# Kernel tuning notes

Hardware: AMD Instinct MI355X
Metric: run time of the kernel (lower is better)

The kernel has to match this reference:

```python
import jax, jax.numpy as jnp
import numpy as np

H = 4          # num_heads
DK = 128       # head_k_dim = hidden*expand_k/H = 1024*0.5/4
DV = 256       # head_v_dim = hidden*expand_v/H
LOW_RANK = 16  # gate_low_rank_dim
GATE_NORM = 16.0  # gate_logit_normalizer
CHUNK = 64
EPS = 1e-5


def setup_inputs() -> dict:
    key = jax.random.key(0)
    ks = jax.random.split(key, 10)
    Dm = 1024
    Kd, Vd = H * DK, H * DV  # key_dim=512, value_dim=1024
    def lin(k, fan_in, fan_out):
        return jax.random.normal(k, (fan_in, fan_out), jnp.float32) * (fan_in ** -0.5)
    return {
        "x": jax.random.normal(ks[0], (4, 2048, Dm), jnp.float32),
        "Wq": lin(ks[1], Dm, Kd),
        "Wk": lin(ks[2], Dm, Kd),
        "Wv": lin(ks[3], Dm, Vd),
        "Wg": lin(ks[4], Dm, Vd),            # output gate proj
        "Wgk1": lin(ks[5], Dm, LOW_RANK),     # low-rank gate proj (no bias)
        "Wgk2": lin(ks[6], LOW_RANK, Kd),     # second gate proj (with bias)
        "bgk2": jnp.zeros((Kd,), jnp.float32),
        "Wo": lin(ks[7], Vd, Dm),
        "gnw": jnp.ones((DV,), jnp.float32),  # FusedRMSNormGated weight
    }


def _gla_chunk(q, k, v, gk):
    """Exact chunkwise evaluation of the GLA recurrence:
       S_t = diag(exp(gk_t)) S_{t-1} + k_t^T v_t;  o_t = scale * q_t S_t.
       q,k,gk: [B,T,H,DK], v: [B,T,H,DV]."""
    B, T, _, _ = q.shape
    NC, C = T // CHUNK, CHUNK
    scale = DK ** -0.5
    def chunks(a):  # [B,T,H,D] -> [NC,B,H,C,D]
        return a.reshape(B, NC, C, H, a.shape[-1]).transpose(1, 0, 3, 2, 4)
    qc, kc, vc, gc = chunks(q), chunks(k), chunks(v), chunks(gk)
    G = jnp.cumsum(gc, axis=-2)                    # within-chunk cumulative log-decay
    qg = qc * jnp.exp(G) * scale                   # q_i exp(G_i)
    k_intra = kc * jnp.exp(-G)                     # k_j exp(-G_j)
    kg = kc * jnp.exp(G[..., -1:, :] - G)          # k_j exp(G_C - G_j) for state update
    g_last = jnp.exp(G[..., -1, :])                # exp(G_C): per-chunk total decay
    # intra-chunk causal attention (diagonal included)
    A = jnp.einsum('nbhik,nbhjk->nbhij', qg, k_intra)
    A = jnp.where(jnp.tril(jnp.ones((C, C), bool)), A, 0.0)
    o_intra = jnp.einsum('nbhij,nbhjv->nbhiv', A, vc)
    def step(S, inp):
        qg_, kg_, v_, gl_, oi_ = inp
        o = oi_ + jnp.einsum('bhck,bhkv->bhcv', qg_, S)
        S = S * gl_[..., :, None] + jnp.einsum('bhck,bhcv->bhkv', kg_, v_)
        return S, o
    S0 = jnp.zeros((B, H, DK, DV), q.dtype)
    _, o = jax.lax.scan(step, S0, (qg, kg, vc, g_last, o_intra))
    return o.transpose(1, 0, 3, 2, 4).reshape(B, T, H, DV)


def reference(x, Wq, Wk, Wv, Wg, Wgk1, Wgk2, bgk2, Wo, gnw):
    B, T, Dm = x.shape
    q = (x @ Wq).reshape(B, T, H, DK)
    k = (x @ Wk).reshape(B, T, H, DK)
    v = (x @ Wv).reshape(B, T, H, DV)
    gk = jax.nn.log_sigmoid((x @ Wgk1) @ Wgk2 + bgk2) / GATE_NORM
    gk = gk.reshape(B, T, H, DK)
    o = _gla_chunk(q, k, v, gk)                              # [B,T,H,DV]
    g = (x @ Wg).reshape(B, T, H, DV)
    # FusedRMSNormGated: RMSNorm(o) * weight * swish(g)
    o = o * jax.lax.rsqrt(jnp.mean(o * o, axis=-1, keepdims=True) + EPS) * gnw
    o = o * (g * jax.nn.sigmoid(g))
    return o.reshape(B, T, H * DV) @ Wo
```

## Files before the change

kernel.cpp:

```cpp
#include <hip/hip_runtime.h>
#include <hip/hip_bf16.h>
#include <stdint.h>

#define B_  4
#define T_  2048
#define DM  1024
#define H_  4
#define DK_ 128
#define DV_ 256
#define KD  512
#define VD  1024
#define NCH 32
#define CC  64
#define BT  8192
#define SCALE 0.08838834764831845f
#define GNORM_INV 0.0625f

typedef __attribute__((ext_vector_type(8))) short short8;
typedef __attribute__((ext_vector_type(4))) float f32x4;
typedef uint32_t u32;
typedef unsigned short ushort_t;

__device__ inline ushort_t f2b(float f) {
    u32 u = __builtin_bit_cast(u32, f);
    u32 r = (u + 0x7fffu + ((u >> 16) & 1u)) >> 16;
    return (ushort_t)r;
}
__device__ inline void unpack2(u32 u, float& lo, float& hi) {
    lo = __builtin_bit_cast(float, u << 16);
    hi = __builtin_bit_cast(float, u & 0xffff0000u);
}
__device__ inline void gload_lds16(const void* g, void* l) {
    __builtin_amdgcn_global_load_lds(
        (const __attribute__((address_space(1))) uint32_t*)g,
        (__attribute__((address_space(3))) uint32_t*)l, 16, 0, 0);
}

__global__ __launch_bounds__(256)
void cvtx(const float* __restrict__ x, ushort_t* __restrict__ xb, int n) {
    int idx = (blockIdx.x * 256 + threadIdx.x) * 8;
    if (idx >= n) return;
    float4 a = *(const float4*)&x[idx];
    float4 b = *(const float4*)&x[idx + 4];
    uint4 p;
    p.x = (u32)f2b(a.x) | ((u32)f2b(a.y) << 16);
    p.y = (u32)f2b(a.z) | ((u32)f2b(a.w) << 16);
    p.z = (u32)f2b(b.x) | ((u32)f2b(b.y) << 16);
    p.w = (u32)f2b(b.z) | ((u32)f2b(b.w) << 16);
    *(uint4*)&xb[idx] = p;
}

__global__ __launch_bounds__(256)
void tcvt(const float* __restrict__ W, ushort_t* __restrict__ Wt, int K, int N) {
    __shared__ float tile[32][33];
    const int k0 = blockIdx.x * 32, n0 = blockIdx.y * 32;
    const int r = threadIdx.x >> 3, c4 = (threadIdx.x & 7) * 4;
    float4 wv = *(const float4*)&W[(size_t)(k0 + r) * N + n0 + c4];
    tile[r][c4 + 0] = wv.x; tile[r][c4 + 1] = wv.y;
    tile[r][c4 + 2] = wv.z; tile[r][c4 + 3] = wv.w;
    __syncthreads();
    u32 lo = (u32)f2b(tile[c4 + 0][r]) | ((u32)f2b(tile[c4 + 1][r]) << 16);
    u32 hi = (u32)f2b(tile[c4 + 2][r]) | ((u32)f2b(tile[c4 + 3][r]) << 16);
    uint2 o2; o2.x = lo; o2.y = hi;
    *(uint2*)&Wt[(size_t)(n0 + r) * K + k0 + c4] = o2;
}

__global__ __launch_bounds__(256)
void w1trans(const float* __restrict__ W1, ushort_t* __restrict__ w1t) {
    int idx = blockIdx.x * 256 + threadIdx.x;
    int k = idx >> 4, n = idx & 15;
    w1t[n * 1024 + k] = f2b(W1[k * 16 + n]);
}

__global__ __launch_bounds__(256)
void gemm_qkv(const ushort_t* __restrict__ A, const ushort_t* __restrict__ Bt,
              float* __restrict__ qo, float* __restrict__ ko,
              ushort_t* __restrict__ vo) {
    __shared__ ushort_t Al[128 * 32];
    __shared__ ushort_t Bl[128 * 32];
    const int wg = blockIdx.x;
    const int swz = (wg & 7) * 128 + (wg >> 3);
    const int bx = swz & 63, by = swz >> 6;
    const int t = threadIdx.x;
    const int wave = t >> 6, lane = t & 63;
    const int wr = wave >> 1, wc = wave & 1;
    const int row0 = bx * 128, col0 = by * 128;
    const int lm = lane & 15, lk = (lane >> 4) * 8;

    const int b0 = t * 16;
    const int r0 = b0 >> 6, c0 = (b0 & 63) >> 1;
    const int r1 = (4096 + b0) >> 6, c1 = ((4096 + b0) & 63) >> 1;
    ushort_t* ldsA0 = &Al[(wave * 1024) >> 1];
    ushort_t* ldsA1 = &Al[(4096 + wave * 1024) >> 1];
    ushort_t* ldsB0 = &Bl[(wave * 1024) >> 1];
    ushort_t* ldsB1 = &Bl[(4096 + wave * 1024) >> 1];

    f32x4 acc[4][4];
    #pragma unroll
    for (int i = 0; i < 4; ++i)
        #pragma unroll
        for (int j = 0; j < 4; ++j) acc[i][j] = f32x4{0.f, 0.f, 0.f, 0.f};

    const ushort_t* Ap = A + (size_t)row0 * DM;
    const ushort_t* Bp = Bt + (size_t)col0 * DM;

    for (int k0 = 0; k0 < DM; k0 += 32) {
        __syncthreads();
        gload_lds16(Ap + (size_t)r0 * DM + k0 + c0, ldsA0);
        gload_lds16(Ap + (size_t)r1 * DM + k0 + c1, ldsA1);
        gload_lds16(Bp + (size_t)r0 * DM + k0 + c0, ldsB0);
        gload_lds16(Bp + (size_t)r1 * DM + k0 + c1, ldsB1);
        __syncthreads();
        short8 af[4], bfr[4];
        #pragma unroll
        for (int f = 0; f < 4; ++f)
            af[f] = *(const short8*)(&Al[(wr * 64 + f * 16 + lm) * 32 + lk]);
        #pragma unroll
        for (int f = 0; f < 4; ++f)
            bfr[f] = *(const short8*)(&Bl[(wc * 64 + f * 16 + lm) * 32 + lk]);
        #pragma unroll
        for (int i = 0; i < 4; ++i)
            #pragma unroll
            for (int j = 0; j < 4; ++j)
                acc[i][j] = __builtin_amdgcn_mfma_f32_16x16x32_bf16(af[i], bfr[j], acc[i][j], 0, 0, 0);
    }
    const int orow = row0 + wr * 64 + (lane >> 4) * 4;
    const int cbase = col0 + wc * 64 + lm;
    if (by < 8) {
        float* C = (by < 4) ? qo : ko;
        const int cc0 = cbase - ((by < 4) ? 0 : 512);
        #pragma unroll
        for (int i = 0; i < 4; ++i)
            #pragma unroll
            for (int j = 0; j < 4; ++j)
                #pragma unroll
                for (int e = 0; e < 4; ++e)
                    C[(size_t)(orow + i * 16 + e) * KD + cc0 + j * 16] = acc[i][j][e];
    } else {
        const int cc0 = cbase - 1024;
        #pragma unroll
        for (int i = 0; i < 4; ++i)
            #pragma unroll
            for (int j = 0; j < 4; ++j)
                #pragma unroll
                for (int e = 0; e < 4; ++e)
                    vo[(size_t)(orow + i * 16 + e) * VD + cc0 + j * 16] = f2b(acc[i][j][e]);
    }
}

template<int OUTBF>
__global__ __launch_bounds__(256)
void gemm_bf16(const ushort_t* __restrict__ A, const ushort_t* __restrict__ Bt,
               void* __restrict__ Cout, int M, int N, int K, int nbx) {
    __shared__ ushort_t Al[128 * 32];
    __shared__ ushort_t Bl[128 * 32];
    const int nwg = gridDim.x;
    const int cpx = nwg >> 3;
    const int wg = blockIdx.x;
    const int swz = (wg & 7) * cpx + (wg >> 3);
    const int bx = swz % nbx, by = swz / nbx;
    const int t = threadIdx.x;
    const int wave = t >> 6, lane = t & 63;
    const int wr = wave >> 1, wc = wave & 1;
    const int row0 = bx * 128, col0 = by * 128;
    const int lm = lane & 15, lk = (lane >> 4) * 8;

    const int b0 = t * 16;
    const int r0 = b0 >> 6, c0 = (b0 & 63) >> 1;
    const int r1 = (4096 + b0) >> 6, c1 = ((4096 + b0) & 63) >> 1;
    ushort_t* ldsA0 = &Al[(wave * 1024) >> 1];
    ushort_t* ldsA1 = &Al[(4096 + wave * 1024) >> 1];
    ushort_t* ldsB0 = &Bl[(wave * 1024) >> 1];
    ushort_t* ldsB1 = &Bl[(4096 + wave * 1024) >> 1];

    f32x4 acc[4][4];
    #pragma unroll
    for (int i = 0; i < 4; ++i)
        #pragma unroll
        for (int j = 0; j < 4; ++j) acc[i][j] = f32x4{0.f, 0.f, 0.f, 0.f};

    const ushort_t* Ap = A + (size_t)row0 * K;
    const ushort_t* Bp = Bt + (size_t)col0 * K;

    for (int k0 = 0; k0 < K; k0 += 32) {
        __syncthreads();
        gload_lds16(Ap + (size_t)r0 * K + k0 + c0, ldsA0);
        gload_lds16(Ap + (size_t)r1 * K + k0 + c1, ldsA1);
        gload_lds16(Bp + (size_t)r0 * K + k0 + c0, ldsB0);
        gload_lds16(Bp + (size_t)r1 * K + k0 + c1, ldsB1);
        __syncthreads();
        short8 af[4], bfr[4];
        #pragma unroll
        for (int f = 0; f < 4; ++f)
            af[f] = *(const short8*)(&Al[(wr * 64 + f * 16 + lm) * 32 + lk]);
        #pragma unroll
        for (int f = 0; f < 4; ++f)
            bfr[f] = *(const short8*)(&Bl[(wc * 64 + f * 16 + lm) * 32 + lk]);
        #pragma unroll
        for (int i = 0; i < 4; ++i)
            #pragma unroll
            for (int j = 0; j < 4; ++j)
                acc[i][j] = __builtin_amdgcn_mfma_f32_16x16x32_bf16(af[i], bfr[j], acc[i][j], 0, 0, 0);
    }
    const int orow = row0 + wr * 64 + (lane >> 4) * 4;
    const int ocol = col0 + wc * 64 + lm;
    #pragma unroll
    for (int i = 0; i < 4; ++i)
        #pragma unroll
        for (int j = 0; j < 4; ++j)
            #pragma unroll
            for (int e = 0; e < 4; ++e) {
                int rr = orow + i * 16 + e, cc = ocol + j * 16;
                if (OUTBF) ((ushort_t*)Cout)[(size_t)rr * N + cc] = f2b(acc[i][j][e]);
                else       ((float*)Cout)[(size_t)rr * N + cc]   = acc[i][j][e];
            }
}

__global__ __launch_bounds__(256)
void lowrank_mfma(const ushort_t* __restrict__ xbf, const ushort_t* __restrict__ w1t,
                  float* __restrict__ tmp) {
    const int t = threadIdx.x;
    const int w = t >> 6, lane = t & 63;
    const int lm = lane & 15, lg = lane >> 4;
    const int row0 = blockIdx.x * 64 + w * 16;
    f32x4 acc = {0.f, 0.f, 0.f, 0.f};
    #pragma unroll
    for (int kk = 0; kk < 32; ++kk) {
        short8 a = *(const short8*)&xbf[(size_t)(row0 + lm) * DM + kk * 32 + lg * 8];
        short8 b = *(const short8*)&w1t[(size_t)lm * DM + kk * 32 + lg * 8];
        acc = __builtin_amdgcn_mfma_f32_16x16x32_bf16(a, b, acc, 0, 0, 0);
    }
    #pragma unroll
    for (int e = 0; e < 4; ++e)
        tmp[(size_t)(row0 + lg * 4 + e) * 16 + lm] = acc[e];
}

__global__ __launch_bounds__(256)
void gatek_kernel(const float* __restrict__ tmp, const float* __restrict__ W2,
                  const float* __restrict__ bias, float* __restrict__ gk) {
    const int idx = blockIdx.x * 256 + threadIdx.x;
    const int bt = idx >> 9, c = idx & 511;
    float z = bias[c];
    #pragma unroll
    for (int j = 0; j < 16; ++j)
        z += tmp[bt * 16 + j] * W2[j * KD + c];
    float ls = fminf(z, 0.f) - log1pf(expf(-fabsf(z)));
    gk[idx] = ls * GNORM_INV;
}

__global__ __launch_bounds__(128)
void gateprep_kernel(const float* __restrict__ q, const float* __restrict__ kf,
                     const float* __restrict__ gk,
                     ushort_t* __restrict__ qgb, ushort_t* __restrict__ kib,
                     ushort_t* __restrict__ kgb, float* __restrict__ glast) {
    const int bid = blockIdx.x;
    const int c = bid & 31, bh = bid >> 5;
    const int b = bh >> 2, h = bh & 3;
    const int d = threadIdx.x;
    const int t0 = b * T_ + c * CC;
    const int gbase = t0 * KD + h * DK_ + d;
    const int obase = bid * (CC * DK_) + d;

    float total = 0.f;
    #pragma unroll 8
    for (int i = 0; i < CC; ++i) total += gk[gbase + i * KD];

    float G = 0.f;
    #pragma unroll 4
    for (int i = 0; i < CC; ++i) {
        const int gi = gbase + i * KD;
        G += gk[gi];
        float qv = q[gi], kv = kf[gi];
        qgb[obase + i * DK_] = f2b(qv * expf(G) * SCALE);
        kib[obase + i * DK_] = f2b(kv * expf(-G));
        kgb[obase + i * DK_] = f2b(kv * expf(total - G));
    }
    glast[bid * DK_ + d] = expf(total);
}

__global__ __launch_bounds__(256)
void vtrans_kernel(const ushort_t* __restrict__ vbf, ushort_t* __restrict__ vT) {
    __shared__ ushort_t vl[64][264];
    const int bid = blockIdx.x;
    const int c = bid & 31, bh = bid >> 5;
    const int b = bh >> 2, h = bh & 3;
    const int t0 = b * T_ + c * CC;
    const int t = threadIdx.x;

    #pragma unroll
    for (int m = 0; m < 8; ++m) {
        int p = t + m * 256;
        int j = p >> 5, d8 = (p & 31) * 8;
        *(uint4*)&vl[j][d8] = *(const uint4*)&vbf[(size_t)(t0 + j) * VD + h * DV_ + d8];
    }
    __syncthreads();

    const size_t outb = (size_t)bid * (256 * 64);
    #pragma unroll
    for (int it = 0; it < 2; ++it) {
        int dv = it * 128 + (t >> 1);
        int j0 = (t & 1) * 32;
        u32 vv[16];
        #pragma unroll
        for (int wi = 0; wi < 16; ++wi)
            vv[wi] = (u32)vl[j0 + 2 * wi][dv] | ((u32)vl[j0 + 2 * wi + 1][dv] << 16);
        ushort_t* dst = &vT[outb + (size_t)dv * 64 + j0];
        *(uint4*)(dst + 0)  = make_uint4(vv[0], vv[1], vv[2], vv[3]);
        *(uint4*)(dst + 8)  = make_uint4(vv[4], vv[5], vv[6], vv[7]);
        *(uint4*)(dst + 16) = make_uint4(vv[8], vv[9], vv[10], vv[11]);
        *(uint4*)(dst + 24) = make_uint4(vv[12], vv[13], vv[14], vv[15]);
    }
}

__global__ __launch_bounds__(256)
void chunk_state(const ushort_t* __restrict__ kgb, const ushort_t* __restrict__ vT,
                 ushort_t* __restrict__ Sst) {
    __shared__ ushort_t kgT[128 * 72];
    const int bid = blockIdx.x;
    const int t = threadIdx.x;
    const size_t kgbase = (size_t)bid * (CC * DK_);
    const size_t vtbase = (size_t)bid * (256 * 64);
    const size_t sbase  = (size_t)bid * (256 * 128);

    #pragma unroll
    for (int m = 0; m < 4; ++m) {
        int p = t + m * 256;
        int j = p >> 4, d0 = (p & 15) * 8;
        uint4 r = *(const uint4*)&kgb[kgbase + (size_t)j * DK_ + d0];
        kgT[(d0 + 0) * 72 + j] = (ushort_t)(r.x & 0xffff);
        kgT[(d0 + 1) * 72 + j] = (ushort_t)(r.x >> 16);
        kgT[(d0 + 2) * 72 + j] = (ushort_t)(r.y & 0xffff);
        kgT[(d0 + 3) * 72 + j] = (ushort_t)(r.y >> 16);
        kgT[(d0 + 4) * 72 + j] = (ushort_t)(r.z & 0xffff);
        kgT[(d0 + 5) * 72 + j] = (ushort_t)(r.z >> 16);
        kgT[(d0 + 6) * 72 + j] = (ushort_t)(r.w & 0xffff);
        kgT[(d0 + 7) * 72 + j] = (ushort_t)(r.w >> 16);
    }
    __syncthreads();

    const int w = t >> 6, lane = t & 63;
    const int lm = lane & 15, lg = lane >> 4;
    #pragma unroll
    for (int mm = 0; mm < 4; ++mm) {
        const int mt = w * 4 + mm;
        short8 a0 = *(const short8*)&vT[vtbase + (size_t)(mt * 16 + lm) * 64 + lg * 8];
        short8 a1 = *(const short8*)&vT[vtbase + (size_t)(mt * 16 + lm) * 64 + 32 + lg * 8];
        #pragma unroll
        for (int n = 0; n < 8; ++n) {
            f32x4 acc = {0.f, 0.f, 0.f, 0.f};
            short8 b0 = *(const short8*)&kgT[(n * 16 + lm) * 72 + lg * 8];
            short8 b1 = *(const short8*)&kgT[(n * 16 + lm) * 72 + 32 + lg * 8];
            acc = __builtin_amdgcn_mfma_f32_16x16x32_bf16(a0, b0, acc, 0, 0, 0);
            acc = __builtin_amdgcn_mfma_f32_16x16x32_bf16(a1, b1, acc, 0, 0, 0);
            #pragma unroll
            for (int e = 0; e < 4; ++e)
                Sst[sbase + (size_t)(mt * 16 + lg * 4 + e) * 128 + n * 16 + lm] = f2b(acc[e]);
        }
    }
}

__global__ __launch_bounds__(256)
void scan_combine(ushort_t* __restrict__ Sst, const float* __restrict__ glast) {
    const int bid = blockIdx.x;
    const int dvt = bid & 15, bh = bid >> 4;
    const int t = threadIdx.x;
    const int dv = dvt * 16 + (t >> 4);
    const int dk0 = (t & 15) * 8;

    float P[8];
    #pragma unroll
    for (int e = 0; e < 8; ++e) P[e] = 0.f;

    for (int c = 0; c < NCH; ++c) {
        const size_t base = ((size_t)(bh * NCH + c) * 256 + dv) * 128 + dk0;
        uint4 m0 = *(const uint4*)&Sst[base];
        u32 wd[4];
        #pragma unroll
        for (int e = 0; e < 4; ++e)
            wd[e] = (u32)f2b(P[2 * e]) | ((u32)f2b(P[2 * e + 1]) << 16);
        *(uint4*)&Sst[base] = make_uint4(wd[0], wd[1], wd[2], wd[3]);
        float mv[8];
        unpack2(m0.x, mv[0], mv[1]); unpack2(m0.y, mv[2], mv[3]);
        unpack2(m0.z, mv[4], mv[5]); unpack2(m0.w, mv[6], mv[7]);
        const float* glp = &glast[(size_t)(bh * NCH + c) * DK_ + dk0];
        float4 g0 = *(const float4*)&glp[0];
        float4 g1 = *(const float4*)&glp[4];
        float gl[8] = {g0.x, g0.y, g0.z, g0.w, g1.x, g1.y, g1.z, g1.w};
        #pragma unroll
        for (int e = 0; e < 8; ++e) P[e] = gl[e] * P[e] + mv[e];
    }
}

__global__ __launch_bounds__(256)
void fused_chunk(const ushort_t* __restrict__ qgb, const ushort_t* __restrict__ kib,
                 const ushort_t* __restrict__ vT, const ushort_t* __restrict__ Sst,
                 ushort_t* __restrict__ ob) {
    __shared__ __align__(16) ushort_t lds[24064];
    ushort_t* stg = lds;
    ushort_t* vq  = lds + 10752;
    ushort_t* Al  = lds + 17408;

    const int bid = blockIdx.x;
    const int c = bid & 31, bh = bid >> 5;
    const int b = bh >> 2, h = bh & 3;
    const int t0 = b * T_ + c * CC;
    const int t = threadIdx.x;
    const int w = t >> 6, lane = t & 63;
    const int lm = lane & 15, lg = lane >> 4;
    const int m0 = w * 16;

    const size_t qbase  = (size_t)bid * (CC * DK_);
    const size_t vtbase = (size_t)bid * (256 * 64);
    const size_t sbase  = (size_t)bid * (256 * 128);

    short8 qf[4];
    #pragma unroll
    for (int kk = 0; kk < 4; ++kk)
        qf[kk] = *(const short8*)&qgb[qbase + (size_t)(m0 + lm) * DK_ + kk * 32 + lg * 8];

    #pragma unroll
    for (int m = 0; m < 4; ++m) {
        int p = t + m * 256;
        int j = p >> 4, d0 = (p & 15) * 8;
        *(uint4*)&stg[j * 168 + d0] = *(const uint4*)&kib[qbase + (size_t)j * DK_ + d0];
    }
    __syncthreads();

    f32x4 accA[4];
    #pragma unroll
    for (int jt = 0; jt < 4; ++jt) accA[jt] = f32x4{0.f, 0.f, 0.f, 0.f};
    #pragma unroll
    for (int jt = 0; jt < 4; ++jt)
        #pragma unroll
        for (int kk = 0; kk < 4; ++kk) {
            short8 bfrag = *(const short8*)&stg[(jt * 16 + lm) * 168 + kk * 32 + lg * 8];
            accA[jt] = __builtin_amdgcn_mfma_f32_16x16x32_bf16(qf[kk], bfrag, accA[jt], 0, 0, 0);
        }
    #pragma unroll
    for (int jt = 0; jt < 4; ++jt)
        #pragma unroll
        for (int e = 0; e < 4; ++e) {
            int i = m0 + lg * 4 + e, j = jt * 16 + lm;
            Al[i * 104 + j] = f2b(j <= i ? accA[jt][e] : 0.f);
        }
    __syncthreads();

    short8 af[2];
    #pragma unroll
    for (int kk = 0; kk < 2; ++kk)
        af[kk] = *(const short8*)&Al[(m0 + lm) * 104 + kk * 32 + lg * 8];

    #pragma unroll 1
    for (int qq = 0; qq < 4; ++qq) {
        #pragma unroll
        for (int m = 0; m < 2; ++m) {
            int p = t + m * 256;
            int dvr = p >> 3, d0 = (p & 7) * 8;
            *(uint4*)&vq[dvr * 104 + d0] =
                *(const uint4*)&vT[vtbase + (size_t)(qq * 64 + dvr) * 64 + d0];
        }
        #pragma unroll
        for (int m = 0; m < 4; ++m) {
            int p = t + m * 256;
            int dvr = p >> 4, d0 = (p & 15) * 8;
            *(uint4*)&stg[dvr * 168 + d0] =
                *(const uint4*)&Sst[sbase + (size_t)(qq * 64 + dvr) * 128 + d0];
        }
        __syncthreads();
        #pragma unroll
        for (int n = 0; n < 4; ++n) {
            f32x4 acc = {0.f, 0.f, 0.f, 0.f};
            #pragma unroll
            for (int kk = 0; kk < 2; ++kk) {
                short8 bfrag = *(const short8*)&vq[(n * 16 + lm) * 104 + kk * 32 + lg * 8];
                acc = __builtin_amdgcn_mfma_f32_16x16x32_bf16(af[kk], bfrag, acc, 0, 0, 0);
            }
            #pragma unroll
            for (int kk = 0; kk < 4; ++kk) {
                short8 bfrag = *(const short8*)&stg[(n * 16 + lm) * 168 + kk * 32 + lg * 8];
                acc = __builtin_amdgcn_mfma_f32_16x16x32_bf16(qf[kk], bfrag, acc, 0, 0, 0);
            }
            #pragma unroll
            for (int e = 0; e < 4; ++e)
                ob[(size_t)(t0 + m0 + lg * 4 + e) * VD + h * DV_ + qq * 64 + n * 16 + lm] = f2b(acc[e]);
        }
        __syncthreads();
    }
}

__global__ __launch_bounds__(256)
void normgate_kernel(const ushort_t* __restrict__ ob, const ushort_t* __restrict__ gbf,
                     const float* __restrict__ gnw, ushort_t* __restrict__ obf) {
    const int t = threadIdx.x;
    const int w = t >> 6, lane = t & 63;
    const int row = blockIdx.x * 4 + w;
    const size_t base = (size_t)row * DV_ + lane * 4;

    uint2 ov2 = *(const uint2*)&ob[base];
    float o0v, o1v, o2v, o3v;
    unpack2(ov2.x, o0v, o1v); unpack2(ov2.y, o2v, o3v);
    float ssq = o0v * o0v + o1v * o1v + o2v * o2v + o3v * o3v;
    #pragma unroll
    for (int off = 32; off > 0; off >>= 1) ssq += __shfl_xor(ssq, off);
    const float rms = rsqrtf(ssq * (1.0f / DV_) + 1e-5f);

    uint2 gv2 = *(const uint2*)&gbf[base];
    float g0, g1, g2, g3;
    unpack2(gv2.x, g0, g1); unpack2(gv2.y, g2, g3);
    float4 wv = *(const float4*)&gnw[lane * 4];
    float r0 = o0v * rms * wv.x * (g0 / (1.f + expf(-g0)));
    float r1 = o1v * rms * wv.y * (g1 / (1.f + expf(-g1)));
    float r2 = o2v * rms * wv.z * (g2 / (1.f + expf(-g2)));
    float r3 = o3v * rms * wv.w * (g3 / (1.f + expf(-g3)));
    uint2 p;
    p.x = (u32)f2b(r0) | ((u32)f2b(r1) << 16);
    p.y = (u32)f2b(r2) | ((u32)f2b(r3) << 16);
    *(uint2*)&obf[base] = p;
}

extern "C" void kernel_launch(void* const* d_in, const int* in_sizes, int n_in,
                              void* d_out, int out_size, void* d_ws, size_t ws_size,
                              hipStream_t stream) {
    const float* x    = (const float*)d_in[0];
    const float* Wq   = (const float*)d_in[1];
    const float* Wk   = (const float*)d_in[2];
    const float* Wv   = (const float*)d_in[3];
    const float* Wg   = (const float*)d_in[4];
    const float* Wgk1 = (const float*)d_in[5];
    const float* Wgk2 = (const float*)d_in[6];
    const float* bgk2 = (const float*)d_in[7];
    const float* Wo   = (const float*)d_in[8];
    const float* gnw  = (const float*)d_in[9];

    float* ws = (float*)d_ws;
    float* q       = ws;
    float* kf      = ws + 4194304;
    float* gk      = ws + 8388608;
    ushort_t* vT   = (ushort_t*)(ws + 12582912);
    ushort_t* Sst  = (ushort_t*)(ws + 16777216);
    ushort_t* vbf  = (ushort_t*)(ws + 16777216);
    ushort_t* wcat = (ushort_t*)(ws + 20971520);
    ushort_t* wgt  = (ushort_t*)(ws + 22020096);
    ushort_t* obf  = (ushort_t*)(ws + 16777216);
    ushort_t* wbfO = (ushort_t*)(ws + 20971520);
    ushort_t* ob   = (ushort_t*)ws;
    ushort_t* gbf  = (ushort_t*)(ws + 4194304);
    ushort_t* xbf  = (ushort_t*)(ws + 25165824);
    ushort_t* qgb  = (ushort_t*)(ws + 29360128);
    ushort_t* kib  = (ushort_t*)(ws + 31457280);
    ushort_t* kgb  = (ushort_t*)(ws + 33554432);
    float* tmp16   = ws + 35651584;
    float* glast   = ws + 35782656;
    ushort_t* w1t  = (ushort_t*)(ws + 35848192);

    cvtx<<<4096, 256, 0, stream>>>(x, xbf, BT * DM);
    w1trans<<<64, 256, 0, stream>>>(Wgk1, w1t);

    tcvt<<<dim3(32, 16), 256, 0, stream>>>(Wq, wcat, DM, KD);
    tcvt<<<dim3(32, 16), 256, 0, stream>>>(Wk, wcat + (size_t)512 * 1024, DM, KD);
    tcvt<<<dim3(32, 32), 256, 0, stream>>>(Wv, wcat + (size_t)1024 * 1024, DM, VD);
    tcvt<<<dim3(32, 32), 256, 0, stream>>>(Wg, wgt, DM, VD);

    gemm_qkv<<<1024, 256, 0, stream>>>(xbf, wcat, q, kf, vbf);

    lowrank_mfma<<<128, 256, 0, stream>>>(xbf, w1t, tmp16);
    gatek_kernel<<<16384, 256, 0, stream>>>(tmp16, Wgk2, bgk2, gk);
    gateprep_kernel<<<512, 128, 0, stream>>>(q, kf, gk, qgb, kib, kgb, glast);

    gemm_bf16<1><<<512, 256, 0, stream>>>(xbf, wgt, gbf, BT, VD, DM, 64);

    vtrans_kernel<<<512, 256, 0, stream>>>(vbf, vT);
    chunk_state<<<512, 256, 0, stream>>>(kgb, vT, Sst);
    scan_combine<<<256, 256, 0, stream>>>(Sst, glast);
    fused_chunk<<<512, 256, 0, stream>>>(qgb, kib, vT, Sst, ob);

    tcvt<<<dim3(32, 32), 256, 0, stream>>>(Wo, wbfO, VD, DM);
    normgate_kernel<<<8192, 256, 0, stream>>>(ob, gbf, gnw, obf);
    gemm_bf16<0><<<512, 256, 0, stream>>>(obf, wbfO, (float*)d_out, BT, DM, VD, 64);
}
```

Baseline: 360.1 us.

## Fuse gate projection into gateprep and store q/k/v as one bf16 buffer

Removes the separate gatek kernel: gateprep now loads the low-rank tmp16 rows into LDS and recomputes the log-sigmoid gate per element, once for the chunk total and once for the cumulative sum. The QKV GEMM now writes a single bf16 [BT,2048] buffer instead of fp32 q/k plus bf16 v. Together these cut the fp32 gk write and read and halve q/k traffic. The GEMM tile mapping is changed to an XCD-aware block assignment with hardcoded dimensions, and the workspace layout and launch order are rearranged so the buffers that now alias are consumed before they are overwritten. In exchange, q and k are rounded to bf16 earlier, and the gate arithmetic is done twice per element.

```diff
diff --git a/kernel.cpp b/kernel.cpp
--- a/kernel.cpp
+++ b/kernel.cpp
@@ -26,6 +26,9 @@
     u32 r = (u + 0x7fffu + ((u >> 16) & 1u)) >> 16;
     return (ushort_t)r;
 }
+__device__ inline float b2f(ushort_t h) {
+    return __builtin_bit_cast(float, (u32)h << 16);
+}
 __device__ inline void unpack2(u32 u, float& lo, float& hi) {
     lo = __builtin_bit_cast(float, u << 16);
     hi = __builtin_bit_cast(float, u & 0xffff0000u);
@@ -74,13 +77,13 @@
 
 __global__ __launch_bounds__(256)
 void gemm_qkv(const ushort_t* __restrict__ A, const ushort_t* __restrict__ Bt,
-              float* __restrict__ qo, float* __restrict__ ko,
-              ushort_t* __restrict__ vo) {
+              ushort_t* __restrict__ qkvo) {
     __shared__ ushort_t Al[128 * 32];
     __shared__ ushort_t Bl[128 * 32];
     const int wg = blockIdx.x;
-    const int swz = (wg & 7) * 128 + (wg >> 3);
-    const int bx = swz & 63, by = swz >> 6;
+    const int xcd = wg & 7, local = wg >> 3;
+    const int bx = (xcd & 3) * 16 + (local & 15);
+    const int by = (xcd >> 2) * 8 + (local >> 4);
     const int t = threadIdx.x;
     const int wave = t >> 6, lane = t & 63;
     const int wr = wave >> 1, wc = wave & 1;
@@ -125,40 +128,26 @@
                 acc[i][j] = __builtin_amdgcn_mfma_f32_16x16x32_bf16(af[i], bfr[j], acc[i][j], 0, 0, 0);
     }
     const int orow = row0 + wr * 64 + (lane >> 4) * 4;
-    const int cbase = col0 + wc * 64 + lm;
-    if (by < 8) {
-        float* C = (by < 4) ? qo : ko;
-        const int cc0 = cbase - ((by < 4) ? 0 : 512);
-        #pragma unroll
-        for (int i = 0; i < 4; ++i)
-            #pragma unroll
-            for (int j = 0; j < 4; ++j)
-                #pragma unroll
-                for (int e = 0; e < 4; ++e)
-                    C[(size_t)(orow + i * 16 + e) * KD + cc0 + j * 16] = acc[i][j][e];
-    } else {
-        const int cc0 = cbase - 1024;
-        #pragma unroll
-        for (int i = 0; i < 4; ++i)
-            #pragma unroll
-            for (int j = 0; j < 4; ++j)
-                #pragma unroll
-                for (int e = 0; e < 4; ++e)
-                    vo[(size_t)(orow + i * 16 + e) * VD + cc0 + j * 16] = f2b(acc[i][j][e]);
-    }
+    const int ocol = col0 + wc * 64 + lm;
+    #pragma unroll
+    for (int i = 0; i < 4; ++i)
+        #pragma unroll
+        for (int j = 0; j < 4; ++j)
+            #pragma unroll
+            for (int e = 0; e < 4; ++e)
+                qkvo[(size_t)(orow + i * 16 + e) * 2048 + ocol + j * 16] = f2b(acc[i][j][e]);
 }
 
 template<int OUTBF>
 __global__ __launch_bounds__(256)
 void gemm_bf16(const ushort_t* __restrict__ A, const ushort_t* __restrict__ Bt,
-               void* __restrict__ Cout, int M, int N, int K, int nbx) {
+               void* __restrict__ Cout) {
     __shared__ ushort_t Al[128 * 32];
     __shared__ ushort_t Bl[128 * 32];
-    const int nwg = gridDim.x;
-    const int cpx = nwg >> 3;
     const int wg = blockIdx.x;
-    const int swz = (wg & 7) * cpx + (wg >> 3);
-    const int bx = swz % nbx, by = swz / nbx;
+    const int xcd = wg & 7, local = wg >> 3;
+    const int bx = (xcd & 3) * 16 + (local & 15);
+    const int by = (xcd >> 2) * 4 + (local >> 4);
     const int t = threadIdx.x;
     const int wave = t >> 6, lane = t & 63;
     const int wr = wave >> 1, wc = wave & 1;
@@ -179,15 +168,15 @@
         #pragma unroll
         for (int j = 0; j < 4; ++j) acc[i][j] = f32x4{0.f, 0.f, 0.f, 0.f};
 
-    const ushort_t* Ap = A + (size_t)row0 * K;
-    const ushort_t* Bp = Bt + (size_t)col0 * K;
-
-    for (int k0 = 0; k0 < K; k0 += 32) {
+    const ushort_t* Ap = A + (size_t)row0 * DM;
+    const ushort_t* Bp = Bt + (size_t)col0 * DM;
+
+    for (int k0 = 0; k0 < DM; k0 += 32) {
         __syncthreads();
-        gload_lds16(Ap + (size_t)r0 * K + k0 + c0, ldsA0);
-        gload_lds16(Ap + (size_t)r1 * K + k0 + c1, ldsA1);
-        gload_lds16(Bp + (size_t)r0 * K + k0 + c0, ldsB0);
-        gload_lds16(Bp + (size_t)r1 * K + k0 + c1, ldsB1);
+        gload_lds16(Ap + (size_t)r0 * DM + k0 + c0, ldsA0);
+        gload_lds16(Ap + (size_t)r1 * DM + k0 + c1, ldsA1);
+        gload_lds16(Bp + (size_t)r0 * DM + k0 + c0, ldsB0);
+        gload_lds16(Bp + (size_t)r1 * DM + k0 + c1, ldsB1);
         __syncthreads();
         short8 af[4], bfr[4];
         #pragma unroll
@@ -211,8 +200,8 @@
             #pragma unroll
             for (int e = 0; e < 4; ++e) {
                 int rr = orow + i * 16 + e, cc = ocol + j * 16;
-                if (OUTBF) ((ushort_t*)Cout)[(size_t)rr * N + cc] = f2b(acc[i][j][e]);
-                else       ((float*)Cout)[(size_t)rr * N + cc]   = acc[i][j][e];
+                if (OUTBF) ((ushort_t*)Cout)[(size_t)rr * 1024 + cc] = f2b(acc[i][j][e]);
+                else       ((float*)Cout)[(size_t)rr * 1024 + cc]   = acc[i][j][e];
             }
 }
 
@@ -235,42 +224,50 @@
         tmp[(size_t)(row0 + lg * 4 + e) * 16 + lm] = acc[e];
 }
 
-__global__ __launch_bounds__(256)
-void gatek_kernel(const float* __restrict__ tmp, const float* __restrict__ W2,
-                  const float* __restrict__ bias, float* __restrict__ gk) {
-    const int idx = blockIdx.x * 256 + threadIdx.x;
-    const int bt = idx >> 9, c = idx & 511;
-    float z = bias[c];
-    #pragma unroll
-    for (int j = 0; j < 16; ++j)
-        z += tmp[bt * 16 + j] * W2[j * KD + c];
-    float ls = fminf(z, 0.f) - log1pf(expf(-fabsf(z)));
-    gk[idx] = ls * GNORM_INV;
-}
-
 __global__ __launch_bounds__(128)
-void gateprep_kernel(const float* __restrict__ q, const float* __restrict__ kf,
-                     const float* __restrict__ gk,
+void gateprep_kernel(const ushort_t* __restrict__ qkv, const float* __restrict__ tmp16,
+                     const float* __restrict__ W2, const float* __restrict__ bias,
                      ushort_t* __restrict__ qgb, ushort_t* __restrict__ kib,
                      ushort_t* __restrict__ kgb, float* __restrict__ glast) {
+    __shared__ float sm[64][16];
     const int bid = blockIdx.x;
     const int c = bid & 31, bh = bid >> 5;
     const int b = bh >> 2, h = bh & 3;
     const int d = threadIdx.x;
     const int t0 = b * T_ + c * CC;
-    const int gbase = t0 * KD + h * DK_ + d;
+    const int cg = h * DK_ + d;
     const int obase = bid * (CC * DK_) + d;
 
+    #pragma unroll
+    for (int m = 0; m < 2; ++m) {
+        int idx = d + m * 128;
+        int row = idx >> 2, col4 = (idx & 3) * 4;
+        *(float4*)&sm[row][col4] = *(const float4*)&tmp16[(size_t)(t0 + row) * 16 + col4];
+    }
+    __syncthreads();
+
+    float w2c[16];
+    #pragma unroll
+    for (int j = 0; j < 16; ++j) w2c[j] = W2[j * KD + cg];
+    const float bs = bias[cg];
+
     float total = 0.f;
-    #pragma unroll 8
-    for (int i = 0; i < CC; ++i) total += gk[gbase + i * KD];
+    for (int i = 0; i < CC; ++i) {
+        float z = bs;
+        #pragma unroll
+        for (int j = 0; j < 16; ++j) z += sm[i][j] * w2c[j];
+        total += (fminf(z, 0.f) - log1pf(expf(-fabsf(z)))) * GNORM_INV;
+    }
 
     float G = 0.f;
-    #pragma unroll 4
     for (int i = 0; i < CC; ++i) {
-        const int gi = gbase + i * KD;
-        G += gk[gi];
-        float qv = q[gi], kv = kf[gi];
+        float z = bs;
+        #pragma unroll
+        for (int j = 0; j < 16; ++j) z += sm[i][j] * w2c[j];
+        G += (fminf(z, 0.f) - log1pf(expf(-fabsf(z)))) * GNORM_INV;
+        const size_t qrow = (size_t)(t0 + i) * 2048;
+        float qv = b2f(qkv[qrow + cg]);
+        float kv = b2f(qkv[qrow + 512 + cg]);
         qgb[obase + i * DK_] = f2b(qv * expf(G) * SCALE);
         kib[obase + i * DK_] = f2b(kv * expf(-G));
         kgb[obase + i * DK_] = f2b(kv * expf(total - G));
@@ -279,7 +276,7 @@
 }
 
 __global__ __launch_bounds__(256)
-void vtrans_kernel(const ushort_t* __restrict__ vbf, ushort_t* __restrict__ vT) {
+void vtrans_kernel(const ushort_t* __restrict__ qkv, ushort_t* __restrict__ vT) {
     __shared__ ushort_t vl[64][264];
     const int bid = blockIdx.x;
     const int c = bid & 31, bh = bid >> 5;
@@ -291,7 +288,8 @@
     for (int m = 0; m < 8; ++m) {
         int p = t + m * 256;
         int j = p >> 5, d8 = (p & 31) * 8;
-        *(uint4*)&vl[j][d8] = *(const uint4*)&vbf[(size_t)(t0 + j) * VD + h * DV_ + d8];
+        *(uint4*)&vl[j][d8] =
+            *(const uint4*)&qkv[(size_t)(t0 + j) * 2048 + 1024 + h * DV_ + d8];
     }
     __syncthreads();
 
@@ -533,25 +531,22 @@
     const float* gnw  = (const float*)d_in[9];
 
     float* ws = (float*)d_ws;
-    float* q       = ws;
-    float* kf      = ws + 4194304;
-    float* gk      = ws + 8388608;
-    ushort_t* vT   = (ushort_t*)(ws + 12582912);
-    ushort_t* Sst  = (ushort_t*)(ws + 16777216);
-    ushort_t* vbf  = (ushort_t*)(ws + 16777216);
-    ushort_t* wcat = (ushort_t*)(ws + 20971520);
-    ushort_t* wgt  = (ushort_t*)(ws + 22020096);
-    ushort_t* obf  = (ushort_t*)(ws + 16777216);
-    ushort_t* wbfO = (ushort_t*)(ws + 20971520);
+    ushort_t* qkv  = (ushort_t*)ws;
     ushort_t* ob   = (ushort_t*)ws;
     ushort_t* gbf  = (ushort_t*)(ws + 4194304);
-    ushort_t* xbf  = (ushort_t*)(ws + 25165824);
-    ushort_t* qgb  = (ushort_t*)(ws + 29360128);
-    ushort_t* kib  = (ushort_t*)(ws + 31457280);
-    ushort_t* kgb  = (ushort_t*)(ws + 33554432);
-    float* tmp16   = ws + 35651584;
-    float* glast   = ws + 35782656;
-    ushort_t* w1t  = (ushort_t*)(ws + 35848192);
+    ushort_t* vT   = (ushort_t*)(ws + 8388608);
+    ushort_t* Sst  = (ushort_t*)(ws + 12582912);
+    ushort_t* wcat = (ushort_t*)(ws + 12582912);
+    ushort_t* wgt  = (ushort_t*)(ws + 13631488);
+    ushort_t* obf  = (ushort_t*)(ws + 12582912);
+    ushort_t* wbfO = (ushort_t*)(ws + 16777216);
+    ushort_t* xbf  = (ushort_t*)(ws + 20971520);
+    ushort_t* qgb  = (ushort_t*)(ws + 25165824);
+    ushort_t* kib  = (ushort_t*)(ws + 27262976);
+    ushort_t* kgb  = (ushort_t*)(ws + 29360128);
+    float* tmp16   = ws + 31457280;
+    float* glast   = ws + 31588352;
+    ushort_t* w1t  = (ushort_t*)(ws + 31653888);
 
     cvtx<<<4096, 256, 0, stream>>>(x, xbf, BT * DM);
     w1trans<<<64, 256, 0, stream>>>(Wgk1, w1t);
@@ -561,20 +556,20 @@
     tcvt<<<dim3(32, 32), 256, 0, stream>>>(Wv, wcat + (size_t)1024 * 1024, DM, VD);
     tcvt<<<dim3(32, 32), 256, 0, stream>>>(Wg, wgt, DM, VD);
 
-    gemm_qkv<<<1024, 256, 0, stream>>>(xbf, wcat, q, kf, vbf);
+    gemm_qkv<<<1024, 256, 0, stream>>>(xbf, wcat, qkv);
 
     lowrank_mfma<<<128, 256, 0, stream>>>(xbf, w1t, tmp16);
-    gatek_kernel<<<16384, 256, 0, stream>>>(tmp16, Wgk2, bgk2, gk);
-    gateprep_kernel<<<512, 128, 0, stream>>>(q, kf, gk, qgb, kib, kgb, glast);
-
-    gemm_bf16<1><<<512, 256, 0, stream>>>(xbf, wgt, gbf, BT, VD, DM, 64);
-
-    vtrans_kernel<<<512, 256, 0, stream>>>(vbf, vT);
+    gateprep_kernel<<<512, 128, 0, stream>>>(qkv, tmp16, Wgk2, bgk2, qgb, kib, kgb, glast);
+
+    vtrans_kernel<<<512, 256, 0, stream>>>(qkv, vT);
+
+    gemm_bf16<1><<<512, 256, 0, stream>>>(xbf, wgt, gbf);
+
     chunk_state<<<512, 256, 0, stream>>>(kgb, vT, Sst);
     scan_combine<<<256, 256, 0, stream>>>(Sst, glast);
     fused_chunk<<<512, 256, 0, stream>>>(qgb, kib, vT, Sst, ob);
 
     tcvt<<<dim3(32, 32), 256, 0, stream>>>(Wo, wbfO, VD, DM);
     normgate_kernel<<<8192, 256, 0, stream>>>(ob, gbf, gnw, obf);
-    gemm_bf16<0><<<512, 256, 0, stream>>>(obf, wbfO, (float*)d_out, BT, DM, VD, 64);
-}
+    gemm_bf16<0><<<512, 256, 0, stream>>>(obf, wbfO, (float*)d_out);
+}
```

Result: slower. 382.5 us (+6.2%).
